# Kernel tuning notes

Measured on AMD Instinct MI355X. Metric: run time of the kernel, lower is better.

Reference implementation:

```python
import jax, jax.numpy as jnp
import numpy as np

W_BBOX, W_GIOU, W_KPT = 5.0, 2.0, 1.0
EPS_WH = 1e-4  # the module's 0.0001 degenerate-box clamp
B, Q, N, K = 16, 500, 128, 17


def _cxcywh_to_xyxy_clamped(b):
    cx, cy, w, h = b[..., 0], b[..., 1], b[..., 2], b[..., 3]
    x0, y0 = cx - 0.5 * w, cy - 0.5 * h
    x1, y1 = cx + 0.5 * w, cy + 0.5 * h
    x1 = jnp.maximum(x1, x0 + EPS_WH)
    y1 = jnp.maximum(y1, y0 + EPS_WH)
    return jnp.stack([x0, y0, x1, y1], axis=-1)


def _compute_cost(pred_boxes, pred_keypoints, tgt_boxes, tgt_keypoints):
    # L1 bbox cost: (B, Q, N)
    cost_bbox = jnp.sum(jnp.abs(pred_boxes[:, :, None, :] - tgt_boxes[:, None, :, :]), axis=-1)
    # GIoU cost
    p = _cxcywh_to_xyxy_clamped(pred_boxes)   # (B, Q, 4)
    t = _cxcywh_to_xyxy_clamped(tgt_boxes)    # (B, N, 4)
    area_p = (p[..., 2] - p[..., 0]) * (p[..., 3] - p[..., 1])  # (B, Q)
    area_t = (t[..., 2] - t[..., 0]) * (t[..., 3] - t[..., 1])  # (B, N)
    lt = jnp.maximum(p[:, :, None, :2], t[:, None, :, :2])
    rb = jnp.minimum(p[:, :, None, 2:], t[:, None, :, 2:])
    wh = jnp.clip(rb - lt, 0.0)
    inter = wh[..., 0] * wh[..., 1]                              # (B, Q, N)
    union = area_p[:, :, None] + area_t[:, None, :] - inter
    iou = inter / union
    lt_e = jnp.minimum(p[:, :, None, :2], t[:, None, :, :2])
    rb_e = jnp.maximum(p[:, :, None, 2:], t[:, None, :, 2:])
    wh_e = jnp.clip(rb_e - lt_e, 0.0)
    enclose = wh_e[..., 0] * wh_e[..., 1]
    giou = iou - (enclose - union) / enclose
    cost_giou = -giou
    # keypoint L1 cost on flattened 17*2 = 34-dim vectors
    pk = pred_keypoints.reshape(pred_keypoints.shape[0], -1, K * 2)  # (B, Q, 34)
    tk = tgt_keypoints[..., :2].reshape(tgt_keypoints.shape[0], -1, K * 2)  # (B, N, 34)
    cost_kpt = jnp.sum(jnp.abs(pk[:, :, None, :] - tk[:, None, :, :]), axis=-1)
    return W_BBOX * cost_bbox + W_GIOU * cost_giou + W_KPT * cost_kpt


def _lsa(cost):
    # Exact rectangular linear sum assignment (shortest augmenting path / JV),
    # cost: (n, m) with n <= m. Returns col4row: assigned column per row.
    n, m = cost.shape
    u = np.zeros(n)
    v = np.zeros(m)
    col4row = np.full(n, -1, np.int64)
    row4col = np.full(m, -1, np.int64)
    for cur_row in range(n):
        path = np.full(m, -1, np.int64)
        SR = np.zeros(n, bool)
        SC = np.zeros(m, bool)
        spc = np.full(m, np.inf)
        min_val = 0.0
        i = cur_row
        sink = -1
        while sink == -1:
            SR[i] = True
            rem = np.where(~SC)[0]
            r = min_val + cost[i, rem] - u[i] - v[rem]
            upd = r < spc[rem]
            spc[rem[upd]] = r[upd]
            path[rem[upd]] = i
            jmin = rem[np.argmin(spc[rem])]
            min_val = spc[jmin]
            SC[jmin] = True
            if row4col[jmin] == -1:
                sink = jmin
            else:
                i = row4col[jmin]
        u[cur_row] += min_val
        mask = SR.copy()
        mask[cur_row] = False
        u[mask] += min_val - spc[col4row[mask]]
        v[SC] -= min_val - spc[SC]
        j = sink
        while True:
            i = path[j]
            row4col[j] = i
            col4row[i], j = j, col4row[i]
            if i == cur_row:
                break
    return col4row


def _hungarian_batch(cost_np):
    # cost_np: (B, Q, N) with Q >= N. Per-image Hungarian (matches scipy's
    # linear_sum_assignment output ordering: row indices sorted ascending).
    cost_np = np.asarray(cost_np, np.float64)
    b, q, n = cost_np.shape
    rows = np.zeros((b, n), np.int32)
    cols = np.zeros((b, n), np.int32)
    for bi in range(b):
        # transpose so rows (targets) <= cols (queries)
        q4t = _lsa(cost_np[bi].T)  # (N,) query assigned to each target
        order = np.argsort(q4t)
        rows[bi] = q4t[order].astype(np.int32)
        cols[bi] = order.astype(np.int32)
    return rows, cols


def setup_inputs() -> dict:
    key = jax.random.key(0)
    k1, k2, k3, k4 = jax.random.split(key, 4)
    def boxes(k, nb):
        kc, ks = jax.random.split(k)
        cxcy = jax.random.uniform(kc, (B, nb, 2), jnp.float32)
        wh = 0.05 + 0.4 * jax.random.uniform(ks, (B, nb, 2), jnp.float32)
        return jnp.concatenate([cxcy, wh], axis=-1)
    return {
        "pred_boxes": boxes(k1, Q),
        "pred_keypoints": jax.random.uniform(k2, (B, Q, K, 2), jnp.float32),
        "tgt_boxes": boxes(k3, N),
        "tgt_keypoints": jax.random.uniform(k4, (B, N, K, 2), jnp.float32),
    }


def reference(pred_boxes, pred_keypoints, tgt_boxes, tgt_keypoints):
    C = _compute_cost(pred_boxes, pred_keypoints, tgt_boxes, tgt_keypoints)  # (B, Q, N)
    row_ind, col_ind = jax.pure_callback(
        _hungarian_batch,
        (jax.ShapeDtypeStruct((B, N), jnp.int32), jax.ShapeDtypeStruct((B, N), jnp.int32)),
        C,
    )
    return C, row_ind, col_ind
```

## Files before the change

### kernel.cpp

```cpp
#include <hip/hip_runtime.h>
#include <math.h>

#define BB 16
#define QQ 500
#define NN 128
#define KK2 34

__global__ __launch_bounds__(128) void cost_kernel(
    const float* __restrict__ pb,
    const float* __restrict__ pk,
    const float* __restrict__ tb,
    const float* __restrict__ tk,
    float* __restrict__ C,
    float* __restrict__ CT,
    int writeCT)
{
#pragma clang fp contract(off)
    const int q = blockIdx.x;
    const int b = blockIdx.y;
    const int n = threadIdx.x;

    __shared__ float spb[4];
    __shared__ float spk[KK2];
    if (threadIdx.x < 4)
        spb[threadIdx.x] = pb[((size_t)b * QQ + q) * 4 + threadIdx.x];
    if (threadIdx.x < KK2)
        spk[threadIdx.x] = pk[((size_t)b * QQ + q) * KK2 + threadIdx.x];
    __syncthreads();

    const float pcx = spb[0], pcy = spb[1], pw = spb[2], ph = spb[3];

    const size_t tbase = ((size_t)b * NN + n) * 4;
    const float tcx = tb[tbase + 0];
    const float tcy = tb[tbase + 1];
    const float tw  = tb[tbase + 2];
    const float th  = tb[tbase + 3];

    float cb = fabsf(pcx - tcx);
    cb = cb + fabsf(pcy - tcy);
    cb = cb + fabsf(pw - tw);
    cb = cb + fabsf(ph - th);

    float px0 = pcx - 0.5f * pw;
    float py0 = pcy - 0.5f * ph;
    float px1 = pcx + 0.5f * pw;
    float py1 = pcy + 0.5f * ph;
    px1 = fmaxf(px1, px0 + 1e-4f);
    py1 = fmaxf(py1, py0 + 1e-4f);

    float tx0 = tcx - 0.5f * tw;
    float ty0 = tcy - 0.5f * th;
    float tx1 = tcx + 0.5f * tw;
    float ty1 = tcy + 0.5f * th;
    tx1 = fmaxf(tx1, tx0 + 1e-4f);
    ty1 = fmaxf(ty1, ty0 + 1e-4f);

    const float area_p = (px1 - px0) * (py1 - py0);
    const float area_t = (tx1 - tx0) * (ty1 - ty0);

    const float ltx = fmaxf(px0, tx0);
    const float lty = fmaxf(py0, ty0);
    const float rbx = fminf(px1, tx1);
    const float rby = fminf(py1, ty1);
    const float wx = fmaxf(rbx - ltx, 0.0f);
    const float wy = fmaxf(rby - lty, 0.0f);
    const float inter = wx * wy;
    const float uni = (area_p + area_t) - inter;
    const float iou = inter / uni;

    const float ex0 = fminf(px0, tx0);
    const float ey0 = fminf(py0, ty0);
    const float ex1 = fmaxf(px1, tx1);
    const float ey1 = fmaxf(py1, ty1);
    const float ewx = fmaxf(ex1 - ex0, 0.0f);
    const float ewy = fmaxf(ey1 - ey0, 0.0f);
    const float enc = ewx * ewy;

    const float giou = iou - (enc - uni) / enc;
    const float cg = -giou;

    const size_t kbase = ((size_t)b * NN + n) * KK2;
    float ck = 0.0f;
    for (int k = 0; k < KK2; ++k)
        ck = ck + fabsf(spk[k] - tk[kbase + k]);

    const float Cv = (5.0f * cb + 2.0f * cg) + ck;

    C[((size_t)b * QQ + q) * NN + n] = Cv;
    if (writeCT)
        CT[((size_t)b * NN + n) * QQ + q] = Cv;
}

__device__ __forceinline__ int rl_i(int v, int l) {
    return __builtin_amdgcn_readlane(v, l);
}
__device__ __forceinline__ double rl_d(double v, int l) {
    int lo = __builtin_amdgcn_readlane(__double2loint(v), l);
    int hi = __builtin_amdgcn_readlane(__double2hiint(v), l);
    return __hiloint2double(hi, lo);
}

template <int CTRL>
__device__ __forceinline__ double dpp_fmin_step(double x) {
    int lo = __double2loint(x);
    int hi = __double2hiint(x);
    int nlo = __builtin_amdgcn_update_dpp(lo, lo, CTRL, 0xF, 0xF, false);
    int nhi = __builtin_amdgcn_update_dpp(hi, hi, CTRL, 0xF, 0xF, false);
    return fmin(__hiloint2double(nhi, nlo), x);
}
#define ROW_SHR1  0x111
#define ROW_SHR2  0x112
#define ROW_SHR4  0x114
#define ROW_SHR8  0x118
#define ROW_BC15  0x142
#define ROW_BC31  0x143

__device__ __forceinline__ double dpp_fmin_wave(double x) {
    x = dpp_fmin_step<ROW_SHR1>(x);
    x = dpp_fmin_step<ROW_SHR2>(x);
    x = dpp_fmin_step<ROW_SHR4>(x);
    x = dpp_fmin_step<ROW_SHR8>(x);
    x = dpp_fmin_step<ROW_BC15>(x);
    x = dpp_fmin_step<ROW_BC31>(x);
    return x;
}

#define SEL8(arr, kq, out) do { \
    out = arr[0]; \
    if ((kq)==1) out = arr[1]; if ((kq)==2) out = arr[2]; if ((kq)==3) out = arr[3]; \
    if ((kq)==4) out = arr[4]; if ((kq)==5) out = arr[5]; if ((kq)==6) out = arr[6]; \
    if ((kq)==7) out = arr[7]; } while (0)

#define SCAT8(arr, kq, val) do { \
    if ((kq)==0) arr[0] = (val); if ((kq)==1) arr[1] = (val); \
    if ((kq)==2) arr[2] = (val); if ((kq)==3) arr[3] = (val); \
    if ((kq)==4) arr[4] = (val); if ((kq)==5) arr[5] = (val); \
    if ((kq)==6) arr[6] = (val); if ((kq)==7) arr[7] = (val); } while (0)

__global__ __launch_bounds__(64) void rowmin_kernel(
    const float* __restrict__ CT,
    double* __restrict__ rm)
{
    const int n = blockIdx.x;
    const int b = blockIdx.y;
    const int lane = threadIdx.x;

    const float4* r4 = reinterpret_cast<const float4*>(CT + ((size_t)b * NN + n) * QQ);

    float m = INFINITY;
    int jm = 0;
    {
        float4 a = r4[lane];
        int base = lane * 4;
        if (a.x < m) { m = a.x; jm = base + 0; }
        if (a.y < m) { m = a.y; jm = base + 1; }
        if (a.z < m) { m = a.z; jm = base + 2; }
        if (a.w < m) { m = a.w; jm = base + 3; }
    }
    if (lane < 61) {
        float4 a = r4[64 + lane];
        int base = (64 + lane) * 4;
        if (a.x < m) { m = a.x; jm = base + 0; }
        if (a.y < m) { m = a.y; jm = base + 1; }
        if (a.z < m) { m = a.z; jm = base + 2; }
        if (a.w < m) { m = a.w; jm = base + 3; }
    }

    long long kb = __double_as_longlong((double)m) | (long long)jm;
    double kd = dpp_fmin_wave(__longlong_as_double(kb));
    if (lane == 63)
        rm[(size_t)b * NN + n] = kd;
}

template <bool USE_CT, bool PRE>
__global__ __launch_bounds__(64) void lsa_wave_kernel(
    const float* __restrict__ C,
    const float* __restrict__ CT,
    const double* __restrict__ rm,
    float* __restrict__ out_rows,
    float* __restrict__ out_cols)
{
#pragma clang fp contract(off)
    const int b = blockIdx.x;
    const int lane = threadIdx.x;

    __shared__ double s_spc[64 * 10];
    __shared__ int s_q[NN];

    const float* Cb  = C + (size_t)b * QQ * NN;
    const float* CTb = USE_CT ? (CT + (size_t)b * NN * QQ) : nullptr;

    const int j0 = lane * 8;
    const int nval = (QQ - j0 < 0) ? 0 : ((QQ - j0 > 8) ? 8 : (QQ - j0));

    double v_[8], spc_[8];
    int path_[8], r4c_[8];
    double u0, u1;
    int c4r0 = -1, c4r1 = -1;
    int jm0, jm1;
#pragma unroll
    for (int k = 0; k < 8; ++k) { v_[k] = 0.0; r4c_[k] = -1; }

    if (PRE) {
        const long long p0 = __double_as_longlong(rm[(size_t)b * NN + lane]);
        const long long p1 = __double_as_longlong(rm[(size_t)b * NN + 64 + lane]);
        u0 = __longlong_as_double(p0 & ~0x1FFLL);
        u1 = __longlong_as_double(p1 & ~0x1FFLL);
        jm0 = (int)(p0 & 0x1FF);
        jm1 = (int)(p1 & 0x1FF);
        if (USE_CT) {
            const float4* w4 = reinterpret_cast<const float4*>(CTb);
            float4 acc; acc.x = acc.y = acc.z = acc.w = 0.0f;
#pragma unroll 8
            for (int t = lane; t < (NN * QQ) / 4; t += 64) {
                float4 a = w4[t];
                acc.x += a.x; acc.y += a.y; acc.z += a.z; acc.w += a.w;
            }
            asm volatile("" :: "v"(acc.x), "v"(acc.y), "v"(acc.z), "v"(acc.w));
        }
    } else {
        float m0 = INFINITY, m1 = INFINITY;
        jm0 = 0; jm1 = 0;
#pragma unroll 4
        for (int q = 0; q < QQ; ++q) {
            float a, c;
            if (USE_CT) {
                a = CTb[(size_t)lane * QQ + q];
                c = CTb[(size_t)(64 + lane) * QQ + q];
            } else {
                a = Cb[(size_t)q * NN + lane];
                c = Cb[(size_t)q * NN + 64 + lane];
            }
            if (a < m0) { m0 = a; jm0 = q; }
            if (c < m1) { m1 = c; jm1 = q; }
        }
        u0 = (double)m0;
        u1 = (double)m1;
    }

    for (int i = 0; i < NN; ++i) {
        int jm = (i < 64) ? rl_i(jm0, i) : rl_i(jm1, i - 64);
        int kq = jm & 7;
        int selr; SEL8(r4c_, kq, selr);
        int occ = rl_i(selr, jm >> 3);
        if (occ < 0) {
            if (lane == (jm >> 3)) { SCAT8(r4c_, kq, i); }
            if (i < 64) { if (lane == i) c4r0 = jm; }
            else        { if (lane == i - 64) c4r1 = jm; }
        }
    }

    for (int cur = 0; cur < NN; ++cur) {
        int already = (cur < 64) ? rl_i(c4r0, cur) : rl_i(c4r1, cur - 64);
        if (already >= 0) continue;

        const double INF = INFINITY;
#pragma unroll
        for (int k = 0; k < 8; ++k) { spc_[k] = INF; path_[k] = -1; }
        unsigned int sc = 0;
        int sr0 = 0, sr1 = 0;
        double minv = 0.0;
        int i = cur, sink = -1;

        while (true) {
            float c_[8];
            if (USE_CT) {
                const float4* p = reinterpret_cast<const float4*>(CTb + (size_t)i * QQ + j0);
                if (nval > 0) {
                    float4 a = p[0];
                    c_[0] = a.x; c_[1] = a.y; c_[2] = a.z; c_[3] = a.w;
                } else { c_[0] = c_[1] = c_[2] = c_[3] = 0.0f; }
                if (nval > 4) {
                    float4 a = p[1];
                    c_[4] = a.x; c_[5] = a.y; c_[6] = a.z; c_[7] = a.w;
                } else { c_[4] = c_[5] = c_[6] = c_[7] = 0.0f; }
            } else {
#pragma unroll
                for (int k = 0; k < 8; ++k)
                    c_[k] = (j0 + k < QQ) ? Cb[(size_t)(j0 + k) * NN + i] : 0.0f;
            }

            if (i < 64) { if (lane == i) sr0 = 1; }
            else        { if (lane == i - 64) sr1 = 1; }

            double ui = (i < 64) ? rl_d(u0, i) : rl_d(u1, i - 64);
            double s = minv - ui;

#pragma unroll
            for (int k = 0; k < 8; ++k) {
                double r = (s + (double)c_[k]) - v_[k];
                long long rb = (__double_as_longlong(r) & ~0x1FFLL)
                             | (long long)(j0 + k);
                double rp = __longlong_as_double(rb);
                bool ok = (k < nval) && !((sc >> k) & 1) && (rp < spc_[k]);
                if (ok) { spc_[k] = rp; path_[k] = i; }
            }

            double val[8];
#pragma unroll
            for (int k = 0; k < 8; ++k) {
                bool okk = (k < nval) && !((sc >> k) & 1);
                val[k] = okk ? spc_[k] : INF;
            }
            double t01 = fmin(val[0], val[1]);
            double t23 = fmin(val[2], val[3]);
            double t45 = fmin(val[4], val[5]);
            double t67 = fmin(val[6], val[7]);
            double lmin = fmin(fmin(t01, t23), fmin(t45, t67));

            double gk = rl_d(dpp_fmin_wave(lmin), 63);

            int jmin   = (int)(__double_as_longlong(gk) & 0x1FFLL);
            int winner = jmin >> 3;

            if (lane == winner) sc |= 1u << (jmin & 7);

            int kq = jmin & 7;
            int selr; SEL8(r4c_, kq, selr);
            int r4 = rl_i(selr, winner);

            minv = gk;
            if (r4 < 0) { sink = jmin; break; }
            i = r4;
        }

        {
            double* base = s_spc + lane * 10;
            double2 d01; d01.x = spc_[0]; d01.y = spc_[1];
            double2 d23; d23.x = spc_[2]; d23.y = spc_[3];
            double2 d45; d45.x = spc_[4]; d45.y = spc_[5];
            double2 d67; d67.x = spc_[6]; d67.y = spc_[7];
            *(double2*)(base + 0) = d01;
            *(double2*)(base + 2) = d23;
            *(double2*)(base + 4) = d45;
            *(double2*)(base + 6) = d67;
        }
        __syncthreads();
        const int g0i = (c4r0 < 0) ? 0 : c4r0;
        const int g1i = (c4r1 < 0) ? 0 : c4r1;
        const double g0 = s_spc[(g0i >> 3) * 10 + (g0i & 7)];
        const double g1 = s_spc[(g1i >> 3) * 10 + (g1i & 7)];

        if (lane == cur) { u0 = u0 + minv; }
        else if (sr0)    { double t = minv - g0; u0 = u0 + t; }
        if (lane + 64 == cur) { u1 = u1 + minv; }
        else if (sr1)         { double t = minv - g1; u1 = u1 + t; }
#pragma unroll
        for (int k = 0; k < 8; ++k) {
            if ((k < nval) && ((sc >> k) & 1)) {
                double t = minv - spc_[k];
                v_[k] = v_[k] - t;
            }
        }
        __syncthreads();

        int j = sink;
        while (true) {
            int kq = j & 7, src = j >> 3;
            int sp; SEL8(path_, kq, sp);
            int i2 = rl_i(sp, src);
            if (lane == src) { SCAT8(r4c_, kq, i2); }
            int t2;
            if (i2 < 64) {
                t2 = rl_i(c4r0, i2);
                if (lane == i2) c4r0 = j;
            } else {
                t2 = rl_i(c4r1, i2 - 64);
                if (lane == i2 - 64) c4r1 = j;
            }
            j = t2;
            if (i2 == cur) break;
        }
    }

    s_q[lane] = c4r0;
    s_q[64 + lane] = c4r1;
    __syncthreads();
    int rank0 = 0, rank1 = 0;
    for (int t = 0; t < NN; ++t) {
        int qv = s_q[t];
        rank0 += (qv < c4r0) ? 1 : 0;
        rank1 += (qv < c4r1) ? 1 : 0;
    }
    out_rows[(size_t)b * NN + rank0] = (float)c4r0;
    out_cols[(size_t)b * NN + rank0] = (float)lane;
    out_rows[(size_t)b * NN + rank1] = (float)c4r1;
    out_cols[(size_t)b * NN + rank1] = (float)(64 + lane);
}

extern "C" void kernel_launch(void* const* d_in, const int* in_sizes, int n_in,
                              void* d_out, int out_size, void* d_ws, size_t ws_size,
                              hipStream_t stream) {
    const float* pb = (const float*)d_in[0];
    const float* pk = (const float*)d_in[1];
    const float* tb = (const float*)d_in[2];
    const float* tk = (const float*)d_in[3];

    float* outC  = (float*)d_out;
    float* orows = outC + (size_t)BB * QQ * NN;
    float* ocols = orows + (size_t)BB * NN;

    const size_t ct_bytes = (size_t)BB * NN * QQ * sizeof(float);
    const size_t rm_bytes = (size_t)BB * NN * sizeof(double);
    const bool useCT = (ws_size >= ct_bytes);
    const bool pre   = (ws_size >= ct_bytes + rm_bytes);
    float*  CT = useCT ? (float*)d_ws : nullptr;
    double* RM = pre ? (double*)((char*)d_ws + ct_bytes) : nullptr;

    dim3 grid(QQ, BB);
    cost_kernel<<<grid, 128, 0, stream>>>(pb, pk, tb, tk, outC, CT, useCT ? 1 : 0);

    if (pre) {
        rowmin_kernel<<<dim3(NN, BB), 64, 0, stream>>>(CT, RM);
        lsa_wave_kernel<true, true><<<BB, 64, 0, stream>>>(outC, CT, RM, orows, ocols);
    } else if (useCT) {
        lsa_wave_kernel<true, false><<<BB, 64, 0, stream>>>(outC, CT, nullptr, orows, ocols);
    } else {
        lsa_wave_kernel<false, false><<<BB, 64, 0, stream>>>(outC, nullptr, nullptr, orows, ocols);
    }
}
```

Measured before the change: 129.3 us.

## Add auction-style augmenting row reduction before shortest-path augmentation

Inserts a Jonker-Volgenant augmenting row reduction phase after the greedy column-min initialization. Free rows bid for their best column using the top-two reduced costs, found by wave-wide min reductions. The winning column's dual is lowered, and any displaced row is chained as the next bidder, capped at 192 steps. This aims to assign most rows cheaply, so fewer expensive Dijkstra-style augmentations run in the later loop. It adds serial steps and relies on the later loop's correctness under the modified duals.

```diff
diff --git a/kernel.cpp b/kernel.cpp
--- a/kernel.cpp
+++ b/kernel.cpp
@@ -250,6 +250,75 @@
         }
     }
 
+    if (USE_CT) {
+        unsigned long long fr0 = __ballot(c4r0 < 0);
+        unsigned long long fr1 = __ballot(c4r1 < 0);
+        int steps = 0;
+        int i = -1;
+        while (steps < 192) {
+            if (i < 0) {
+                if (fr0)      { i = __ffsll((long long)fr0) - 1; fr0 &= fr0 - 1; }
+                else if (fr1) { i = 64 + (__ffsll((long long)fr1) - 1); fr1 &= fr1 - 1; }
+                else break;
+            }
+            ++steps;
+            float c_[8];
+            {
+                const float4* p = reinterpret_cast<const float4*>(CTb + (size_t)i * QQ + j0);
+                if (nval > 0) { float4 a = p[0]; c_[0]=a.x; c_[1]=a.y; c_[2]=a.z; c_[3]=a.w; }
+                else { c_[0]=c_[1]=c_[2]=c_[3]=0.0f; }
+                if (nval > 4) { float4 a = p[1]; c_[4]=a.x; c_[5]=a.y; c_[6]=a.z; c_[7]=a.w; }
+                else { c_[4]=c_[5]=c_[6]=c_[7]=0.0f; }
+            }
+            double m1 = INFINITY, m2 = INFINITY; int jl = 0;
+#pragma unroll
+            for (int k = 0; k < 8; ++k) {
+                double t = (k < nval) ? ((double)c_[k] - v_[k]) : INFINITY;
+                bool lt1 = t < m1;
+                m2 = lt1 ? m1 : fmin(m2, t);
+                jl = lt1 ? (j0 + k) : jl;
+                m1 = lt1 ? t : m1;
+            }
+            double g1 = rl_d(dpp_fmin_wave(m1), 63);
+            unsigned long long bl = __ballot(m1 == g1);
+            int winner = __ffsll((long long)bl) - 1;
+            int j1 = rl_i(jl, winner);
+            double a2 = (lane == winner) ? m2 : m1;
+            double g2 = rl_d(dpp_fmin_wave(a2), 63);
+            int kq = j1 & 7;
+            int selr; SEL8(r4c_, kq, selr);
+            int i0 = rl_i(selr, j1 >> 3);
+
+            if (g1 < g2) {
+                if (i < 64) { if (lane == i) { u0 = g2; c4r0 = j1; } }
+                else        { if (lane == i - 64) { u1 = g2; c4r1 = j1; } }
+                if (lane == (j1 >> 3)) {
+                    double vv; SEL8(v_, kq, vv);
+                    vv = vv - (g2 - g1);
+                    SCAT8(v_, kq, vv);
+                    SCAT8(r4c_, kq, i);
+                }
+                if (i0 >= 0) {
+                    if (i0 < 64) { if (lane == i0) c4r0 = -1; }
+                    else         { if (lane == i0 - 64) c4r1 = -1; }
+                    i = i0;
+                } else {
+                    i = -1;
+                }
+            } else {
+                if (i0 < 0) {
+                    if (i < 64) { if (lane == i) { u0 = g1; c4r0 = j1; } }
+                    else        { if (lane == i - 64) { u1 = g1; c4r1 = j1; } }
+                    if (lane == (j1 >> 3)) { SCAT8(r4c_, kq, i); }
+                } else {
+                    if (i < 64) { if (lane == i) u0 = g1; }
+                    else        { if (lane == i - 64) u1 = g1; }
+                }
+                i = -1;
+            }
+        }
+    }
+
     for (int cur = 0; cur < NN; ++cur) {
         int already = (cur < 64) ? rl_i(c4r0, cur) : rl_i(c4r1, cur - 64);
         if (already >= 0) continue;
```

New measurement: 128.3 us (median of 2 runs). About the same (-0.7%).

## Store transposed cost matrix as double to skip per-iteration conversions in LSA

Applied to the files above, without the earlier changes.

The cost kernel now writes the transposed cost matrix as doubles when the workspace is large enough, and a new double-precision row-min kernel reads that copy. The LSA kernel then loads doubles directly, so it no longer converts float to double in the augmenting loop. Padding columns are filled with INF, which removes the per-element nval checks, and several __syncthreads barriers are dropped because the kernel runs as a single wave. In exchange it doubles transpose-write and read traffic, and relies on single-wave LDS ordering without barriers.

```diff
diff --git a/kernel.cpp b/kernel.cpp
--- a/kernel.cpp
+++ b/kernel.cpp
@@ -12,8 +12,9 @@
     const float* __restrict__ tb,
     const float* __restrict__ tk,
     float* __restrict__ C,
-    float* __restrict__ CT,
-    int writeCT)
+    float* __restrict__ CTF,
+    double* __restrict__ CTD,
+    int wf32, int wf64)
 {
 #pragma clang fp contract(off)
     const int q = blockIdx.x;
@@ -87,8 +88,10 @@
     const float Cv = (5.0f * cb + 2.0f * cg) + ck;
 
     C[((size_t)b * QQ + q) * NN + n] = Cv;
-    if (writeCT)
-        CT[((size_t)b * NN + n) * QQ + q] = Cv;
+    if (wf32)
+        CTF[((size_t)b * NN + n) * QQ + q] = Cv;
+    if (wf64)
+        CTD[((size_t)b * NN + n) * QQ + q] = (double)Cv;
 }
 
 __device__ __forceinline__ int rl_i(int v, int l) {
@@ -137,15 +140,15 @@
     if ((kq)==4) arr[4] = (val); if ((kq)==5) arr[5] = (val); \
     if ((kq)==6) arr[6] = (val); if ((kq)==7) arr[7] = (val); } while (0)
 
-__global__ __launch_bounds__(64) void rowmin_kernel(
-    const float* __restrict__ CT,
+__global__ __launch_bounds__(64) void rowmin32_kernel(
+    const float* __restrict__ CTF,
     double* __restrict__ rm)
 {
     const int n = blockIdx.x;
     const int b = blockIdx.y;
     const int lane = threadIdx.x;
 
-    const float4* r4 = reinterpret_cast<const float4*>(CT + ((size_t)b * NN + n) * QQ);
+    const float4* r4 = reinterpret_cast<const float4*>(CTF + ((size_t)b * NN + n) * QQ);
 
     float m = INFINITY;
     int jm = 0;
@@ -172,10 +175,39 @@
         rm[(size_t)b * NN + n] = kd;
 }
 
-template <bool USE_CT, bool PRE>
+__global__ __launch_bounds__(64) void rowmin64_kernel(
+    const double* __restrict__ CTD,
+    double* __restrict__ rm)
+{
+    const int n = blockIdx.x;
+    const int b = blockIdx.y;
+    const int lane = threadIdx.x;
+
+    const double2* r2 = reinterpret_cast<const double2*>(CTD + ((size_t)b * NN + n) * QQ);
+
+    double m = INFINITY;
+    int jm = 0;
+#pragma unroll
+    for (int t = 0; t < 4; ++t) {
+        int j = lane * 8 + t * 2;
+        if (j + 1 < QQ) {
+            double2 a = r2[lane * 4 + t];
+            if (a.x < m) { m = a.x; jm = j; }
+            if (a.y < m) { m = a.y; jm = j + 1; }
+        }
+    }
+
+    long long kb = __double_as_longlong(m) | (long long)jm;
+    double kd = dpp_fmin_wave(__longlong_as_double(kb));
+    if (lane == 63)
+        rm[(size_t)b * NN + n] = kd;
+}
+
+template <int MODE, bool PRE>
 __global__ __launch_bounds__(64) void lsa_wave_kernel(
     const float* __restrict__ C,
-    const float* __restrict__ CT,
+    const float* __restrict__ CTF,
+    const double* __restrict__ CTD,
     const double* __restrict__ rm,
     float* __restrict__ out_rows,
     float* __restrict__ out_cols)
@@ -187,8 +219,9 @@
     __shared__ double s_spc[64 * 10];
     __shared__ int s_q[NN];
 
-    const float* Cb  = C + (size_t)b * QQ * NN;
-    const float* CTb = USE_CT ? (CT + (size_t)b * NN * QQ) : nullptr;
+    const float*  Cb   = C + (size_t)b * QQ * NN;
+    const float*  CTFb = (MODE == 1) ? (CTF + (size_t)b * NN * QQ) : nullptr;
+    const double* CTDb = (MODE == 2) ? (CTD + (size_t)b * NN * QQ) : nullptr;
 
     const int j0 = lane * 8;
     const int nval = (QQ - j0 < 0) ? 0 : ((QQ - j0 > 8) ? 8 : (QQ - j0));
@@ -208,8 +241,16 @@
         u1 = __longlong_as_double(p1 & ~0x1FFLL);
         jm0 = (int)(p0 & 0x1FF);
         jm1 = (int)(p1 & 0x1FF);
-        if (USE_CT) {
-            const float4* w4 = reinterpret_cast<const float4*>(CTb);
+        if (MODE == 2) {
+            const double2* w2 = reinterpret_cast<const double2*>(CTDb);
+            double acc = 0.0;
+            for (int t = lane; t < (NN * QQ) / 2; t += 64) {
+                double2 a = w2[t];
+                acc += a.x + a.y;
+            }
+            asm volatile("" :: "v"(acc));
+        } else if (MODE == 1) {
+            const float4* w4 = reinterpret_cast<const float4*>(CTFb);
             float4 acc; acc.x = acc.y = acc.z = acc.w = 0.0f;
 #pragma unroll 8
             for (int t = lane; t < (NN * QQ) / 4; t += 64) {
@@ -224,9 +265,9 @@
 #pragma unroll 4
         for (int q = 0; q < QQ; ++q) {
             float a, c;
-            if (USE_CT) {
-                a = CTb[(size_t)lane * QQ + q];
-                c = CTb[(size_t)(64 + lane) * QQ + q];
+            if (MODE == 1) {
+                a = CTFb[(size_t)lane * QQ + q];
+                c = CTFb[(size_t)(64 + lane) * QQ + q];
             } else {
                 a = Cb[(size_t)q * NN + lane];
                 c = Cb[(size_t)q * NN + 64 + lane];
@@ -263,21 +304,33 @@
         int i = cur, sink = -1;
 
         while (true) {
-            float c_[8];
-            if (USE_CT) {
-                const float4* p = reinterpret_cast<const float4*>(CTb + (size_t)i * QQ + j0);
+            double c_[8];
+            if (MODE == 2) {
+                const double2* p = reinterpret_cast<const double2*>(CTDb + (size_t)i * QQ + j0);
+                if (nval > 0) {
+                    double2 a = p[0], b2 = p[1];
+                    c_[0] = a.x; c_[1] = a.y; c_[2] = b2.x; c_[3] = b2.y;
+                } else { c_[0] = c_[1] = c_[2] = c_[3] = INF; }
+                if (nval > 4) {
+                    double2 a = p[2], b2 = p[3];
+                    c_[4] = a.x; c_[5] = a.y; c_[6] = b2.x; c_[7] = b2.y;
+                } else { c_[4] = c_[5] = c_[6] = c_[7] = INF; }
+            } else if (MODE == 1) {
+                const float4* p = reinterpret_cast<const float4*>(CTFb + (size_t)i * QQ + j0);
                 if (nval > 0) {
                     float4 a = p[0];
-                    c_[0] = a.x; c_[1] = a.y; c_[2] = a.z; c_[3] = a.w;
-                } else { c_[0] = c_[1] = c_[2] = c_[3] = 0.0f; }
+                    c_[0] = (double)a.x; c_[1] = (double)a.y;
+                    c_[2] = (double)a.z; c_[3] = (double)a.w;
+                } else { c_[0] = c_[1] = c_[2] = c_[3] = INF; }
                 if (nval > 4) {
                     float4 a = p[1];
-                    c_[4] = a.x; c_[5] = a.y; c_[6] = a.z; c_[7] = a.w;
-                } else { c_[4] = c_[5] = c_[6] = c_[7] = 0.0f; }
+                    c_[4] = (double)a.x; c_[5] = (double)a.y;
+                    c_[6] = (double)a.z; c_[7] = (double)a.w;
+                } else { c_[4] = c_[5] = c_[6] = c_[7] = INF; }
             } else {
 #pragma unroll
                 for (int k = 0; k < 8; ++k)
-                    c_[k] = (j0 + k < QQ) ? Cb[(size_t)(j0 + k) * NN + i] : 0.0f;
+                    c_[k] = (j0 + k < QQ) ? (double)Cb[(size_t)(j0 + k) * NN + i] : INF;
             }
 
             if (i < 64) { if (lane == i) sr0 = 1; }
@@ -288,20 +341,18 @@
 
 #pragma unroll
             for (int k = 0; k < 8; ++k) {
-                double r = (s + (double)c_[k]) - v_[k];
+                double r = (s + c_[k]) - v_[k];
                 long long rb = (__double_as_longlong(r) & ~0x1FFLL)
                              | (long long)(j0 + k);
                 double rp = __longlong_as_double(rb);
-                bool ok = (k < nval) && !((sc >> k) & 1) && (rp < spc_[k]);
+                bool ok = !((sc >> k) & 1) && (rp < spc_[k]);
                 if (ok) { spc_[k] = rp; path_[k] = i; }
             }
 
             double val[8];
 #pragma unroll
-            for (int k = 0; k < 8; ++k) {
-                bool okk = (k < nval) && !((sc >> k) & 1);
-                val[k] = okk ? spc_[k] : INF;
-            }
+            for (int k = 0; k < 8; ++k)
+                val[k] = ((sc >> k) & 1) ? INF : spc_[k];
             double t01 = fmin(val[0], val[1]);
             double t23 = fmin(val[2], val[3]);
             double t45 = fmin(val[4], val[5]);
@@ -335,7 +386,6 @@
             *(double2*)(base + 4) = d45;
             *(double2*)(base + 6) = d67;
         }
-        __syncthreads();
         const int g0i = (c4r0 < 0) ? 0 : c4r0;
         const int g1i = (c4r1 < 0) ? 0 : c4r1;
         const double g0 = s_spc[(g0i >> 3) * 10 + (g0i & 7)];
@@ -347,12 +397,11 @@
         else if (sr1)         { double t = minv - g1; u1 = u1 + t; }
 #pragma unroll
         for (int k = 0; k < 8; ++k) {
-            if ((k < nval) && ((sc >> k) & 1)) {
+            if ((sc >> k) & 1) {
                 double t = minv - spc_[k];
                 v_[k] = v_[k] - t;
             }
         }
-        __syncthreads();
 
         int j = sink;
         while (true) {
@@ -375,7 +424,6 @@
 
     s_q[lane] = c4r0;
     s_q[64 + lane] = c4r1;
-    __syncthreads();
     int rank0 = 0, rank1 = 0;
     for (int t = 0; t < NN; ++t) {
         int qv = s_q[t];
@@ -400,22 +448,30 @@
     float* orows = outC + (size_t)BB * QQ * NN;
     float* ocols = orows + (size_t)BB * NN;
 
-    const size_t ct_bytes = (size_t)BB * NN * QQ * sizeof(float);
-    const size_t rm_bytes = (size_t)BB * NN * sizeof(double);
-    const bool useCT = (ws_size >= ct_bytes);
-    const bool pre   = (ws_size >= ct_bytes + rm_bytes);
-    float*  CT = useCT ? (float*)d_ws : nullptr;
-    double* RM = pre ? (double*)((char*)d_ws + ct_bytes) : nullptr;
+    const size_t ctd_bytes = (size_t)BB * NN * QQ * sizeof(double);
+    const size_t ctf_bytes = (size_t)BB * NN * QQ * sizeof(float);
+    const size_t rm_bytes  = (size_t)BB * NN * sizeof(double);
 
     dim3 grid(QQ, BB);
-    cost_kernel<<<grid, 128, 0, stream>>>(pb, pk, tb, tk, outC, CT, useCT ? 1 : 0);
-
-    if (pre) {
-        rowmin_kernel<<<dim3(NN, BB), 64, 0, stream>>>(CT, RM);
-        lsa_wave_kernel<true, true><<<BB, 64, 0, stream>>>(outC, CT, RM, orows, ocols);
-    } else if (useCT) {
-        lsa_wave_kernel<true, false><<<BB, 64, 0, stream>>>(outC, CT, nullptr, orows, ocols);
+
+    if (ws_size >= ctd_bytes + rm_bytes) {
+        double* CTD = (double*)d_ws;
+        double* RM  = (double*)((char*)d_ws + ctd_bytes);
+        cost_kernel<<<grid, 128, 0, stream>>>(pb, pk, tb, tk, outC, nullptr, CTD, 0, 1);
+        rowmin64_kernel<<<dim3(NN, BB), 64, 0, stream>>>(CTD, RM);
+        lsa_wave_kernel<2, true><<<BB, 64, 0, stream>>>(outC, nullptr, CTD, RM, orows, ocols);
+    } else if (ws_size >= ctf_bytes + rm_bytes) {
+        float*  CTF = (float*)d_ws;
+        double* RM  = (double*)((char*)d_ws + ctf_bytes);
+        cost_kernel<<<grid, 128, 0, stream>>>(pb, pk, tb, tk, outC, CTF, nullptr, 1, 0);
+        rowmin32_kernel<<<dim3(NN, BB), 64, 0, stream>>>(CTF, RM);
+        lsa_wave_kernel<1, true><<<BB, 64, 0, stream>>>(outC, CTF, nullptr, RM, orows, ocols);
+    } else if (ws_size >= ctf_bytes) {
+        float* CTF = (float*)d_ws;
+        cost_kernel<<<grid, 128, 0, stream>>>(pb, pk, tb, tk, outC, CTF, nullptr, 1, 0);
+        lsa_wave_kernel<1, false><<<BB, 64, 0, stream>>>(outC, CTF, nullptr, nullptr, orows, ocols);
     } else {
-        lsa_wave_kernel<false, false><<<BB, 64, 0, stream>>>(outC, nullptr, nullptr, orows, ocols);
-    }
-}
+        cost_kernel<<<grid, 128, 0, stream>>>(pb, pk, tb, tk, outC, nullptr, nullptr, 0, 0);
+        lsa_wave_kernel<0, false><<<BB, 64, 0, stream>>>(outC, nullptr, nullptr, nullptr, orows, ocols);
+    }
+}
```

After: 230.5 us. +78.3%, slower.
